# Performance work log

Measured on AMD Instinct MI355X. Metric: run time of the kernel, lower is better.

Reference implementation:

```python
import jax, jax.numpy as jnp
import numpy as np

B = 8
INPUT_SHAPE = (32, 32, 32)
N = int(np.prod(INPUT_SHAPE))  # 32768
K = 128


def setup_inputs() -> dict:
    key = jax.random.key(0)
    k1, k2, k3, k4 = jax.random.split(key, 4)
    data = jax.random.normal(k1, (B,) + INPUT_SHAPE, dtype=jnp.float32)
    mask = jax.random.uniform(k2, (B,) + INPUT_SHAPE, dtype=jnp.float32)
    mult = jax.random.normal(k3, (N, K), dtype=jnp.float32) * 0.05  # RandomNormal init
    sigma_sq = jax.random.normal(k4, (1,), dtype=jnp.float32) * 0.05
    return {"data": data, "mask": mask, "mult": mult, "sigma_sq": sigma_sq}


def reference(data, mask, mult, sigma_sq):
    # Two-arg branch of SpatiallySparseDense_old.call (a_fact == 1).
    b = data.shape[0]
    n, k = mult.shape
    data_flat = data.reshape(b, n)          # [B, N]
    mask_flat = mask.reshape(b, n)          # [B, N]
    # W0 = mask_flat * mult, per batch: [B, N, K]
    W0 = mask_flat[:, :, None] * mult[None, :, :]
    # Gram matrix W0^T W0 + sigma^2 * I : [B, K, K]
    gram = jnp.einsum('bnk,bnl->bkl', W0, W0)
    seye = sigma_sq[0] * jnp.eye(k, dtype=data.dtype)
    pre = jnp.linalg.inv(gram + seye[None])  # [B, K, K] (matches tf.linalg.inv)
    # m = W0^T data : [B, K, 1]
    m = jnp.einsum('bnk,bn->bk', W0, data_flat)[..., None]
    res = jnp.matmul(pre, m)                # [B, K, 1]
    return res
```

## Files before the change

kernel.cpp:

```cpp
#include <hip/hip_runtime.h>

#define BATCH 8
#define NN 32768
#define KK 128
#define NCHUNK 64
#define CHUNK 512
#define NST 8
#define NITER 8

typedef __attribute__((ext_vector_type(8)))  _Float16 half8;
typedef __attribute__((ext_vector_type(4)))  _Float16 half4;
typedef __attribute__((ext_vector_type(16))) float    f32x16;

#define MT_OFF   0ull
#define WH_OFF   (MT_OFF + 8388608ull)
#define DH_OFF   (WH_OFF + 524288ull)
#define GP_OFF   (DH_OFF + 524288ull)
#define MP_OFF   (GP_OFF + 10485760ull)
#define G_OFF    (MP_OFF + 262144ull)

__global__ __launch_bounds__(256) void prep_kernel(
    const float* __restrict__ data, const float* __restrict__ mask,
    const float* __restrict__ mult, unsigned char* __restrict__ ws)
{
    __shared__ _Float16 t[128][136];
    const int tid = threadIdx.x;
    const int n0  = blockIdx.x * 128;

    {
        const int b = tid >> 5, q = tid & 31;
        const size_t src = (size_t)b * NN + n0 + q * 4;
        const float4 d4 = *(const float4*)(data + src);
        const float4 m4 = *(const float4*)(mask + src);
        half4 w = { (_Float16)m4.x, (_Float16)m4.y, (_Float16)m4.z, (_Float16)m4.w };
        half4 d = { (_Float16)d4.x, (_Float16)d4.y, (_Float16)d4.z, (_Float16)d4.w };
        *(half4*)((_Float16*)(ws + WH_OFF) + src) = w;
        *(half4*)((_Float16*)(ws + DH_OFF) + src) = d;
    }

    const float4* m4p = (const float4*)mult;
#pragma unroll
    for (int u = 0; u < 16; ++u) {
        const int c16 = u * 256 + tid;
        const int n  = c16 >> 5;
        const int kq = c16 & 31;
        float4 v = m4p[(size_t)(n0 + n) * 32 + kq];
        half4 h = { (_Float16)v.x, (_Float16)v.y, (_Float16)v.z, (_Float16)v.w };
        const int c4s = kq ^ ((n >> 3) & 7);
        *(half4*)&t[n][c4s * 4] = h;
    }
    __syncthreads();

    _Float16* mt = (_Float16*)(ws + MT_OFF);
    const int g = tid & 15;
#pragma unroll
    for (int i = 0; i < 8; ++i) {
        const int k = (tid >> 4) + i * 16;
        half8 v;
#pragma unroll
        for (int j = 0; j < 8; ++j) {
            const int n = g * 8 + j;
            const int cs = (k >> 2) ^ ((n >> 3) & 7);
            v[j] = t[n][cs * 4 + (k & 3)];
        }
        *(half8*)(mt + (size_t)k * NN + n0 + g * 8) = v;
    }
}

__global__ __launch_bounds__(256, 2) void gram_kernel(
    unsigned char* __restrict__ ws)
{
    __shared__ unsigned char smem[36864];
    const int tid = threadIdx.x;
    const int b     = blockIdx.x >> 6;
    const int chunk = blockIdx.x & 63;
    const int n0    = chunk * CHUNK;
    const int w = tid >> 6, l = tid & 63;
    const int hi = l >> 5;

    const _Float16* mt = (const _Float16*)(ws + MT_OFF);

    if (tid < 64) {
        half8 wv = *(const half8*)((const _Float16*)(ws + WH_OFF) + (size_t)b * NN + n0 + tid * 8);
        half8 dv = *(const half8*)((const _Float16*)(ws + DH_OFF) + (size_t)b * NN + n0 + tid * 8);
        *(half8*)(smem + 32768 + tid * 16) = wv;
        *(half8*)(smem + 33792 + tid * 16) = dv;
    }

    const int krow = tid >> 3;
    const int gd   = tid & 7;
    const _Float16* gsrc0 = mt + (size_t)krow * NN + n0 + gd * 8;
    const int wslot = (gd ^ (krow & 7)) * 16;

    uint4 S0, S1, S2, S3;
#define GLOAD(st_) { const _Float16* p = gsrc0 + (size_t)(st_) * 64;          \
        S0 = *(const uint4*)(p);                                              \
        S1 = *(const uint4*)(p + (size_t)32 * NN);                            \
        S2 = *(const uint4*)(p + (size_t)64 * NN);                            \
        S3 = *(const uint4*)(p + (size_t)96 * NN); }
#define DSWRITE(buf_) { unsigned char* bp = smem + (buf_) * 16384 + krow * 128 + wslot; \
        *(uint4*)(bp)         = S0;  *(uint4*)(bp + 4096)  = S1;              \
        *(uint4*)(bp + 8192)  = S2;  *(uint4*)(bp + 12288) = S3; }

    const int frow  = (l & 31) * 128;
    const int fslot = ((w * 2 + hi) ^ (l & 7)) * 16;
    const int wdoff = w * 32 + hi * 16;

    f32x16 a00 = {}, a01 = {}, a02 = {}, a03 = {}, a11 = {},
           a12 = {}, a13 = {}, a22 = {}, a23 = {}, a33 = {};
    float macc0 = 0.f, macc1 = 0.f, macc2 = 0.f, macc3 = 0.f;

    GLOAD(0);
    __syncthreads();
    DSWRITE(0);
    GLOAD(1);
    __syncthreads();

#pragma unroll 2
    for (int st = 0; st < NST; ++st) {
        const int cur = st & 1;
        if (st < NST - 1) {
            DSWRITE(cur ^ 1);
            if (st < NST - 2) GLOAD(st + 2);
        }
        const unsigned char* tb = smem + cur * 16384;
        const half8 wf = *(const half8*)(smem + 32768 + st * 128 + wdoff);
        const half8 df = *(const half8*)(smem + 33792 + st * 128 + wdoff);
        half8 f0 = *(const half8*)(tb +     0 + frow + fslot) * wf;
        half8 f1 = *(const half8*)(tb +  4096 + frow + fslot) * wf;
        half8 f2 = *(const half8*)(tb +  8192 + frow + fslot) * wf;
        half8 f3 = *(const half8*)(tb + 12288 + frow + fslot) * wf;
#pragma unroll
        for (int j = 0; j < 8; ++j) {
            const float dj = (float)df[j];
            macc0 = fmaf((float)f0[j], dj, macc0);
            macc1 = fmaf((float)f1[j], dj, macc1);
            macc2 = fmaf((float)f2[j], dj, macc2);
            macc3 = fmaf((float)f3[j], dj, macc3);
        }
        a00 = __builtin_amdgcn_mfma_f32_32x32x16_f16(f0, f0, a00, 0, 0, 0);
        a01 = __builtin_amdgcn_mfma_f32_32x32x16_f16(f0, f1, a01, 0, 0, 0);
        a02 = __builtin_amdgcn_mfma_f32_32x32x16_f16(f0, f2, a02, 0, 0, 0);
        a03 = __builtin_amdgcn_mfma_f32_32x32x16_f16(f0, f3, a03, 0, 0, 0);
        a11 = __builtin_amdgcn_mfma_f32_32x32x16_f16(f1, f1, a11, 0, 0, 0);
        a12 = __builtin_amdgcn_mfma_f32_32x32x16_f16(f1, f2, a12, 0, 0, 0);
        a13 = __builtin_amdgcn_mfma_f32_32x32x16_f16(f1, f3, a13, 0, 0, 0);
        a22 = __builtin_amdgcn_mfma_f32_32x32x16_f16(f2, f2, a22, 0, 0, 0);
        a23 = __builtin_amdgcn_mfma_f32_32x32x16_f16(f2, f3, a23, 0, 0, 0);
        a33 = __builtin_amdgcn_mfma_f32_32x32x16_f16(f3, f3, a33, 0, 0, 0);
        __syncthreads();
    }

    float* Rb = (float*)smem;
    float* M  = (float*)(smem + 32768);
    _Float16* Gp = (_Float16*)(ws + GP_OFF) + (size_t)(b * NCHUNK + chunk) * 10240;
    float* Mp = (float*)(ws + MP_OFF) + (size_t)(b * NCHUNK + chunk) * KK;

    {
        const int base = (w * 2 + hi) * 128 + (l & 31);
        M[base +  0] = macc0;  M[base + 32] = macc1;
        M[base + 64] = macc2;  M[base + 96] = macc3;
    }

#define WR(A_, r_) {                                                           \
        *(float4*)(Rb + (r_) * 1024 +   0 + l * 4) = make_float4(A_[0],  A_[1],  A_[2],  A_[3]);  \
        *(float4*)(Rb + (r_) * 1024 + 256 + l * 4) = make_float4(A_[4],  A_[5],  A_[6],  A_[7]);  \
        *(float4*)(Rb + (r_) * 1024 + 512 + l * 4) = make_float4(A_[8],  A_[9],  A_[10], A_[11]); \
        *(float4*)(Rb + (r_) * 1024 + 768 + l * 4) = make_float4(A_[12], A_[13], A_[14], A_[15]); }

#define RED(P_)                                                                \
    {                                                                          \
        __syncthreads();                                                       \
        _Pragma("unroll")                                                      \
        for (int pass = 0; pass < 2; ++pass) {                                 \
            const int off = tid * 4;                                           \
            float4 s0 = *(float4*)(Rb + (pass * 4 + 0) * 1024 + off);          \
            float4 s1 = *(float4*)(Rb + (pass * 4 + 1) * 1024 + off);          \
            float4 s2 = *(float4*)(Rb + (pass * 4 + 2) * 1024 + off);          \
            float4 s3 = *(float4*)(Rb + (pass * 4 + 3) * 1024 + off);          \
            half4 hv = { (_Float16)(s0.x + s1.x + s2.x + s3.x),                \
                         (_Float16)(s0.y + s1.y + s2.y + s3.y),                \
                         (_Float16)(s0.z + s1.z + s2.z + s3.z),                \
                         (_Float16)(s0.w + s1.w + s2.w + s3.w) };              \
            *(half4*)(Gp + (2 * (P_) + pass) * 1024 + off) = hv;               \
        }                                                                      \
        if ((P_) == 0 && tid < 128) {                                          \
            float s = 0.f;                                                     \
            _Pragma("unroll")                                                  \
            for (int r8 = 0; r8 < 8; ++r8) s += M[r8 * 128 + tid];             \
            Mp[tid] = s;                                                       \
        }                                                                      \
        __syncthreads();                                                       \
    }

    WR(a00, w) WR(a01, 4 + w)
    RED(0)
    WR(a02, w) WR(a03, 4 + w)
    RED(1)
    WR(a11, w) WR(a12, 4 + w)
    RED(2)
    WR(a13, w) WR(a22, 4 + w)
    RED(3)
    WR(a23, w) WR(a33, 4 + w)
    RED(4)
#undef WR
#undef RED
#undef GLOAD
#undef DSWRITE
}

__global__ __launch_bounds__(256) void reduce_kernel(
    const float* __restrict__ sig, unsigned char* __restrict__ ws)
{
    const int tid = threadIdx.x;
    const int b  = blockIdx.x / 5;
    const int t2 = blockIdx.x % 5;

    const int e_local = tid * 8;
    const int tile = t2 * 2 + (e_local >> 10);
    const int off0 = e_local & 1023;
    const int c2 = off0 >> 8;
    const int l0 = (off0 >> 2) & 63;

    static const int TT[10] = {0,0,0,0,1,1,1,2,2,3};
    static const int UU[10] = {0,1,2,3,1,2,3,2,3,3};
    const int tt = TT[tile], uu = UU[tile];

    const _Float16* Gp = (const _Float16*)(ws + GP_OFF)
                       + (size_t)b * NCHUNK * 10240 + (size_t)t2 * 2048 + e_local;
    float s[8] = {0.f,0.f,0.f,0.f,0.f,0.f,0.f,0.f};
#pragma unroll
    for (int ch = 0; ch < NCHUNK; ++ch) {
        half8 v = *(const half8*)(Gp + (size_t)ch * 10240);
#pragma unroll
        for (int j = 0; j < 8; ++j) s[j] += (float)v[j];
    }

    float* G = (float*)(ws + G_OFF) + (size_t)b * 16384;
    const float sg = sig[0];
#pragma unroll
    for (int j = 0; j < 8; ++j) {
        const int ll = l0 + (j >> 2);
        const int rj = j & 3;
        const int row = rj + 8 * c2 + 4 * (ll >> 5);
        const int col = ll & 31;
        const int Rr = tt * 32 + row;
        const int C  = uu * 32 + col;
        float v = s[j];
        G[Rr * KK + C] = (Rr == C) ? v + sg : v;
        if (tt != uu) G[C * KK + Rr] = v;
    }
}

__device__ __forceinline__ float blockDot4(float a, float bvl, float* red)
{
    float v = a * bvl;
#pragma unroll
    for (int off = 32; off > 0; off >>= 1) v += __shfl_down(v, off, 64);
    const int wid = threadIdx.x >> 6;
    if ((threadIdx.x & 63) == 0) red[wid] = v;
    __syncthreads();
    float s = (red[0] + red[1]) + (red[2] + red[3]);
    __syncthreads();
    return s;
}

__global__ __launch_bounds__(256, 1) void solve_kernel(
    const unsigned char* __restrict__ ws, float* __restrict__ out)
{
    __shared__ float ps[KK];
    __shared__ float qex[256];
    __shared__ float red[4];

    const int tid = threadIdx.x;
    const int b   = blockIdx.x;
    const int i   = tid & 127;
    const int h   = tid >> 7;

    const float* G  = (const float*)(ws + G_OFF) + (size_t)b * 16384;
    const float* Mp = (const float*)(ws + MP_OFF) + (size_t)b * NCHUNK * KK;

    float Gr[64];
#pragma unroll
    for (int j = 0; j < 64; ++j) Gr[j] = G[(size_t)(h * 64 + j) * KK + i];

    float mvv = 0.f;
#pragma unroll
    for (int ch = 0; ch < NCHUNK; ++ch) mvv += Mp[ch * KK + i];

    float x = 0.f, r = mvv, p = r;
    ps[i] = p;
    float rs = blockDot4(r, r, red);

    for (int it = 0; it < NITER; ++it) {
        float q0 = 0.f, q1 = 0.f, q2 = 0.f, q3 = 0.f;
        const float* psh = ps + h * 64;
#pragma unroll
        for (int u = 0; u < 16; ++u) {
            float4 pv = *(const float4*)(psh + 4 * u);
            q0 = fmaf(Gr[4 * u + 0], pv.x, q0);
            q1 = fmaf(Gr[4 * u + 1], pv.y, q1);
            q2 = fmaf(Gr[4 * u + 2], pv.z, q2);
            q3 = fmaf(Gr[4 * u + 3], pv.w, q3);
        }
        qex[tid] = (q0 + q1) + (q2 + q3);
        __syncthreads();
        const float q = qex[i] + qex[128 + i];

        float pq    = blockDot4(p, q, red);
        float alpha = rs / (pq + 1e-30f);
        x = fmaf(alpha, p, x);
        r = fmaf(-alpha, q, r);
        float rs2  = blockDot4(r, r, red);
        float beta = rs2 / (rs + 1e-30f);
        rs = rs2;
        p  = fmaf(beta, p, r);
        __syncthreads();
        ps[i] = p;
        __syncthreads();
    }
    if (h == 0) out[(size_t)b * KK + i] = x;
}

extern "C" void kernel_launch(void* const* d_in, const int* in_sizes, int n_in,
                              void* d_out, int out_size, void* d_ws, size_t ws_size,
                              hipStream_t stream)
{
    const float* data = (const float*)d_in[0];
    const float* mask = (const float*)d_in[1];
    const float* mult = (const float*)d_in[2];
    const float* sig  = (const float*)d_in[3];
    unsigned char* ws = (unsigned char*)d_ws;
    float* out = (float*)d_out;

    prep_kernel  <<<256, 256, 0, stream>>>(data, mask, mult, ws);
    gram_kernel  <<<BATCH * NCHUNK, 256, 0, stream>>>(ws);
    reduce_kernel<<<BATCH * 5, 256, 0, stream>>>(sig, ws);
    solve_kernel <<<BATCH, 256, 0, stream>>>(ws, out);
}
```

Before: 117.5 us.

## Move W0^T data projection into prep kernel and load gram operands directly

The m = W0^T data projection now runs in the prep kernel in fp32, using the staged mult tile and mask*data products. Per-block partials go to a new workspace region, and the reduce kernel sums them so the solve kernel reads one vector. The gram kernel no longer stages mult tiles through LDS with double buffering and barriers. Each lane loads its MFMA operand fragments straight from global memory with register prefetch, which removes the per-step syncthreads and the half-precision data buffer. The risk is less coalesced direct loads (16-byte pieces from 32 rows) and extra work in the prep kernel.

```diff
diff --git a/kernel.cpp b/kernel.cpp
--- a/kernel.cpp
+++ b/kernel.cpp
@@ -13,29 +13,30 @@
 typedef __attribute__((ext_vector_type(16))) float    f32x16;
 
 #define MT_OFF   0ull
-#define WH_OFF   (MT_OFF + 8388608ull)
-#define DH_OFF   (WH_OFF + 524288ull)
-#define GP_OFF   (DH_OFF + 524288ull)
-#define MP_OFF   (GP_OFF + 10485760ull)
-#define G_OFF    (MP_OFF + 262144ull)
+#define WH_OFF   8388608ull
+#define GP_OFF   8912896ull
+#define MP2_OFF  19398656ull
+#define MG_OFF   20447232ull
+#define G_OFF    20451328ull
 
 __global__ __launch_bounds__(256) void prep_kernel(
     const float* __restrict__ data, const float* __restrict__ mask,
     const float* __restrict__ mult, unsigned char* __restrict__ ws)
 {
     __shared__ _Float16 t[128][136];
+    __shared__ float wd[8][128];
     const int tid = threadIdx.x;
     const int n0  = blockIdx.x * 128;
 
     {
-        const int b = tid >> 5, q = tid & 31;
-        const size_t src = (size_t)b * NN + n0 + q * 4;
+        const int bb = tid >> 5, q = tid & 31;
+        const size_t src = (size_t)bb * NN + n0 + q * 4;
         const float4 d4 = *(const float4*)(data + src);
         const float4 m4 = *(const float4*)(mask + src);
-        half4 w = { (_Float16)m4.x, (_Float16)m4.y, (_Float16)m4.z, (_Float16)m4.w };
-        half4 d = { (_Float16)d4.x, (_Float16)d4.y, (_Float16)d4.z, (_Float16)d4.w };
-        *(half4*)((_Float16*)(ws + WH_OFF) + src) = w;
-        *(half4*)((_Float16*)(ws + DH_OFF) + src) = d;
+        half4 wv = { (_Float16)m4.x, (_Float16)m4.y, (_Float16)m4.z, (_Float16)m4.w };
+        *(half4*)((_Float16*)(ws + WH_OFF) + src) = wv;
+        *(float4*)&wd[bb][q * 4] = make_float4(m4.x * d4.x, m4.y * d4.y,
+                                               m4.z * d4.z, m4.w * d4.w);
     }
 
     const float4* m4p = (const float4*)mult;
@@ -65,79 +66,75 @@
         }
         *(half8*)(mt + (size_t)k * NN + n0 + g * 8) = v;
     }
+
+    {
+        const int bb = tid >> 5, kq = tid & 31;
+        float m0 = 0.f, m1 = 0.f, m2 = 0.f, m3 = 0.f;
+#pragma unroll 16
+        for (int nl = 0; nl < 128; ++nl) {
+            const float wdv = wd[bb][nl];
+            const int slot = kq ^ ((nl >> 3) & 7);
+            half4 hv = *(const half4*)&t[nl][slot * 4];
+            m0 = fmaf((float)hv[0], wdv, m0);
+            m1 = fmaf((float)hv[1], wdv, m1);
+            m2 = fmaf((float)hv[2], wdv, m2);
+            m3 = fmaf((float)hv[3], wdv, m3);
+        }
+        float* Mp2 = (float*)(ws + MP2_OFF) + ((size_t)bb * KK + kq * 4) * 256 + blockIdx.x;
+        Mp2[0]   = m0;
+        Mp2[256] = m1;
+        Mp2[512] = m2;
+        Mp2[768] = m3;
+    }
 }
 
 __global__ __launch_bounds__(256, 2) void gram_kernel(
     unsigned char* __restrict__ ws)
 {
-    __shared__ unsigned char smem[36864];
+    __shared__ unsigned char smem[33792];
     const int tid = threadIdx.x;
     const int b     = blockIdx.x >> 6;
     const int chunk = blockIdx.x & 63;
     const int n0    = chunk * CHUNK;
-    const int w = tid >> 6, l = tid & 63;
+    const int w  = tid >> 6;
+    const int l  = tid & 63;
     const int hi = l >> 5;
 
     const _Float16* mt = (const _Float16*)(ws + MT_OFF);
+    _Float16* wls = (_Float16*)(smem + 32768);
 
     if (tid < 64) {
         half8 wv = *(const half8*)((const _Float16*)(ws + WH_OFF) + (size_t)b * NN + n0 + tid * 8);
-        half8 dv = *(const half8*)((const _Float16*)(ws + DH_OFF) + (size_t)b * NN + n0 + tid * 8);
-        *(half8*)(smem + 32768 + tid * 16) = wv;
-        *(half8*)(smem + 33792 + tid * 16) = dv;
-    }
-
-    const int krow = tid >> 3;
-    const int gd   = tid & 7;
-    const _Float16* gsrc0 = mt + (size_t)krow * NN + n0 + gd * 8;
-    const int wslot = (gd ^ (krow & 7)) * 16;
-
-    uint4 S0, S1, S2, S3;
-#define GLOAD(st_) { const _Float16* p = gsrc0 + (size_t)(st_) * 64;          \
-        S0 = *(const uint4*)(p);                                              \
-        S1 = *(const uint4*)(p + (size_t)32 * NN);                            \
-        S2 = *(const uint4*)(p + (size_t)64 * NN);                            \
-        S3 = *(const uint4*)(p + (size_t)96 * NN); }
-#define DSWRITE(buf_) { unsigned char* bp = smem + (buf_) * 16384 + krow * 128 + wslot; \
-        *(uint4*)(bp)         = S0;  *(uint4*)(bp + 4096)  = S1;              \
-        *(uint4*)(bp + 8192)  = S2;  *(uint4*)(bp + 12288) = S3; }
-
-    const int frow  = (l & 31) * 128;
-    const int fslot = ((w * 2 + hi) ^ (l & 7)) * 16;
-    const int wdoff = w * 32 + hi * 16;
+        *(half8*)(wls + tid * 8) = wv;
+    }
+    __syncthreads();
+
+    const _Float16* p0 = mt + (size_t)(l & 31) * NN + n0 + (w * 2 + hi) * 8;
+    const size_t o1 = (size_t)32 * NN, o2 = (size_t)64 * NN, o3 = (size_t)96 * NN;
 
     f32x16 a00 = {}, a01 = {}, a02 = {}, a03 = {}, a11 = {},
            a12 = {}, a13 = {}, a22 = {}, a23 = {}, a33 = {};
-    float macc0 = 0.f, macc1 = 0.f, macc2 = 0.f, macc3 = 0.f;
-
-    GLOAD(0);
-    __syncthreads();
-    DSWRITE(0);
-    GLOAD(1);
-    __syncthreads();
-
-#pragma unroll 2
+
+    half8 F0 = *(const half8*)(p0);
+    half8 F1 = *(const half8*)(p0 + o1);
+    half8 F2 = *(const half8*)(p0 + o2);
+    half8 F3 = *(const half8*)(p0 + o3);
+
+#pragma unroll
     for (int st = 0; st < NST; ++st) {
-        const int cur = st & 1;
+        half8 G0, G1, G2, G3;
         if (st < NST - 1) {
-            DSWRITE(cur ^ 1);
-            if (st < NST - 2) GLOAD(st + 2);
-        }
-        const unsigned char* tb = smem + cur * 16384;
-        const half8 wf = *(const half8*)(smem + 32768 + st * 128 + wdoff);
-        const half8 df = *(const half8*)(smem + 33792 + st * 128 + wdoff);
-        half8 f0 = *(const half8*)(tb +     0 + frow + fslot) * wf;
-        half8 f1 = *(const half8*)(tb +  4096 + frow + fslot) * wf;
-        half8 f2 = *(const half8*)(tb +  8192 + frow + fslot) * wf;
-        half8 f3 = *(const half8*)(tb + 12288 + frow + fslot) * wf;
-#pragma unroll
-        for (int j = 0; j < 8; ++j) {
-            const float dj = (float)df[j];
-            macc0 = fmaf((float)f0[j], dj, macc0);
-            macc1 = fmaf((float)f1[j], dj, macc1);
-            macc2 = fmaf((float)f2[j], dj, macc2);
-            macc3 = fmaf((float)f3[j], dj, macc3);
-        }
+            const _Float16* pn = p0 + (st + 1) * 64;
+            G0 = *(const half8*)(pn);
+            G1 = *(const half8*)(pn + o1);
+            G2 = *(const half8*)(pn + o2);
+            G3 = *(const half8*)(pn + o3);
+        }
+        const half8 wf = *(const half8*)(wls + st * 64 + (w * 2 + hi) * 8);
+        half8 f0 = F0 * wf;
+        half8 f1 = F1 * wf;
+        half8 f2 = F2 * wf;
+        half8 f3 = F3 * wf;
         a00 = __builtin_amdgcn_mfma_f32_32x32x16_f16(f0, f0, a00, 0, 0, 0);
         a01 = __builtin_amdgcn_mfma_f32_32x32x16_f16(f0, f1, a01, 0, 0, 0);
         a02 = __builtin_amdgcn_mfma_f32_32x32x16_f16(f0, f2, a02, 0, 0, 0);
@@ -148,19 +145,11 @@
         a22 = __builtin_amdgcn_mfma_f32_32x32x16_f16(f2, f2, a22, 0, 0, 0);
         a23 = __builtin_amdgcn_mfma_f32_32x32x16_f16(f2, f3, a23, 0, 0, 0);
         a33 = __builtin_amdgcn_mfma_f32_32x32x16_f16(f3, f3, a33, 0, 0, 0);
-        __syncthreads();
+        if (st < NST - 1) { F0 = G0; F1 = G1; F2 = G2; F3 = G3; }
     }
 
     float* Rb = (float*)smem;
-    float* M  = (float*)(smem + 32768);
     _Float16* Gp = (_Float16*)(ws + GP_OFF) + (size_t)(b * NCHUNK + chunk) * 10240;
-    float* Mp = (float*)(ws + MP_OFF) + (size_t)(b * NCHUNK + chunk) * KK;
-
-    {
-        const int base = (w * 2 + hi) * 128 + (l & 31);
-        M[base +  0] = macc0;  M[base + 32] = macc1;
-        M[base + 64] = macc2;  M[base + 96] = macc3;
-    }
 
 #define WR(A_, r_) {                                                           \
         *(float4*)(Rb + (r_) * 1024 +   0 + l * 4) = make_float4(A_[0],  A_[1],  A_[2],  A_[3]);  \
@@ -184,12 +173,6 @@
                          (_Float16)(s0.w + s1.w + s2.w + s3.w) };              \
             *(half4*)(Gp + (2 * (P_) + pass) * 1024 + off) = hv;               \
         }                                                                      \
-        if ((P_) == 0 && tid < 128) {                                          \
-            float s = 0.f;                                                     \
-            _Pragma("unroll")                                                  \
-            for (int r8 = 0; r8 < 8; ++r8) s += M[r8 * 128 + tid];             \
-            Mp[tid] = s;                                                       \
-        }                                                                      \
         __syncthreads();                                                       \
     }
 
@@ -205,8 +188,6 @@
     RED(4)
 #undef WR
 #undef RED
-#undef GLOAD
-#undef DSWRITE
 }
 
 __global__ __launch_bounds__(256) void reduce_kernel(
@@ -250,6 +231,17 @@
         G[Rr * KK + C] = (Rr == C) ? v + sg : v;
         if (tt != uu) G[C * KK + Rr] = v;
     }
+
+    if (t2 == 0 && tid < KK) {
+        const float* src = (const float*)(ws + MP2_OFF) + ((size_t)b * KK + tid) * 256;
+        float msum = 0.f;
+#pragma unroll
+        for (int c = 0; c < 64; ++c) {
+            float4 v = *(const float4*)(src + c * 4);
+            msum += (v.x + v.y) + (v.z + v.w);
+        }
+        ((float*)(ws + MG_OFF))[b * KK + tid] = msum;
+    }
 }
 
 __device__ __forceinline__ float blockDot4(float a, float bvl, float* red)
@@ -277,16 +269,13 @@
     const int i   = tid & 127;
     const int h   = tid >> 7;
 
-    const float* G  = (const float*)(ws + G_OFF) + (size_t)b * 16384;
-    const float* Mp = (const float*)(ws + MP_OFF) + (size_t)b * NCHUNK * KK;
+    const float* G = (const float*)(ws + G_OFF) + (size_t)b * 16384;
 
     float Gr[64];
 #pragma unroll
     for (int j = 0; j < 64; ++j) Gr[j] = G[(size_t)(h * 64 + j) * KK + i];
 
-    float mvv = 0.f;
-#pragma unroll
-    for (int ch = 0; ch < NCHUNK; ++ch) mvv += Mp[ch * KK + i];
+    const float mvv = ((const float*)(ws + MG_OFF))[b * KK + i];
 
     float x = 0.f, r = mvv, p = r;
     ps[i] = p;
```

Measured after the change: 125.1 us. +6.5%, slower.
